# Optimization experiments

Hardware: AMD Instinct MI355X
Metric: run time of the kernel (lower is better)

The kernel has to match this reference:

```python
import jax, jax.numpy as jnp
import numpy as np

NUM_STEPS = 10
T0, T1 = 0.0, 1.0


def setup_inputs() -> dict:
    key = jax.random.key(0)
    ks = jax.random.split(key, 6)
    B, I, H = 4096, 1024, 2048
    sc_ih = 1.0 / np.sqrt(I)
    sc_hh = 1.0 / np.sqrt(H)
    return {
        "x": jax.random.normal(ks[0], (B, I), jnp.float32),
        "h0": jax.random.normal(ks[1], (B, H), jnp.float32),
        "W_ih": jax.random.normal(ks[2], (H, I), jnp.float32) * sc_ih,
        "b_ih": jax.random.normal(ks[3], (H,), jnp.float32) * sc_ih,
        "W_hh": jax.random.normal(ks[4], (H, H), jnp.float32) * sc_hh,
        "b_hh": jax.random.normal(ks[5], (H,), jnp.float32) * sc_hh,
        "tau": jnp.ones((H,), jnp.float32),
    }


def reference(x, h0, W_ih, b_ih, W_hh, b_hh, tau):
    dt = (T1 - T0) / NUM_STEPS
    # time-invariant input drive: W_ih(input) is the same every step
    ih = x @ W_ih.T + b_ih  # [B, H]
    decay = jnp.exp(-dt / tau)  # [H]

    def step(h, _):
        pre = ih + h @ W_hh.T + b_hh
        target = jnp.tanh(pre)
        h_new = decay * h + (1.0 - decay) * target
        return h_new, None

    h_final, _ = jax.lax.scan(step, h0, None, length=NUM_STEPS)
    return h_final
```

## Files before the change

### kernel.cpp

```cpp
#include <hip/hip_runtime.h>
#include <hip/hip_bf16.h>

#define NUM_STEPS 10
#define DT 0.1f

typedef __bf16 bf16_t;
typedef __bf16 bf16x8 __attribute__((ext_vector_type(8)));
typedef __bf16 bf16x4 __attribute__((ext_vector_type(4)));
typedef float f32x4 __attribute__((ext_vector_type(4)));

__device__ __forceinline__ void async16(const bf16_t* g, bf16_t* l) {
  __builtin_amdgcn_global_load_lds(
      (const __attribute__((address_space(1))) void*)g,
      (__attribute__((address_space(3))) void*)l, 16, 0, 0);
}

__global__ void cvt_f32_to_bf16(const float* __restrict__ in,
                                bf16_t* __restrict__ out, int n4) {
  int i = blockIdx.x * blockDim.x + threadIdx.x;
  if (i < n4) {
    float4 v = ((const float4*)in)[i];
    bf16x4 o = {(bf16_t)v.x, (bf16_t)v.y, (bf16_t)v.z, (bf16_t)v.w};
    ((bf16x4*)out)[i] = o;
  }
}

__global__ void make_decay(const float* __restrict__ tau,
                           float* __restrict__ decay, int n) {
  int i = blockIdx.x * blockDim.x + threadIdx.x;
  if (i < n) decay[i] = __expf(-DT / tau[i]);
}

template <int EPI>
__global__ __launch_bounds__(512, 2) void gemm_nt(
    const bf16_t* __restrict__ A, const bf16_t* __restrict__ Bw, int M, int N,
    int K, const float* __restrict__ bias1, const float* __restrict__ bias2,
    bf16_t* __restrict__ out_ihb, const bf16_t* __restrict__ ihb,
    const float* __restrict__ decay, const bf16_t* __restrict__ hb_prev,
    bf16_t* __restrict__ hb_next, float* __restrict__ out_f32, int writeOut) {
  extern __shared__ char smem[];

  const int tid = threadIdx.x;
  const int lane = tid & 63;
  const int wave = tid >> 6;
  const int waveM = wave >> 1;
  const int waveN = wave & 1;

  const int lin = blockIdx.y * gridDim.x + blockIdx.x;
  const int xcd = lin & 7;
  const int slot = lin >> 3;
  const int bx = (xcd & 1) * 8 + (slot & 7);
  const int by = (xcd >> 1) * 4 + (slot >> 3);
  const long bRow = (long)by * 256;
  const long bCol = (long)bx * 128;

  const int laneRow = lane & 15;
  const int laneK = (lane >> 4) << 3;
  const bf16_t* aG0 = A + (bRow + (wave * 2 + 0) * 16 + laneRow) * (long)K + laneK;
  const bf16_t* aG1 = A + (bRow + (wave * 2 + 1) * 16 + laneRow) * (long)K + laneK;
  const bf16_t* bG = Bw + (bCol + wave * 16 + laneRow) * (long)K + laneK;

  f32x4 acc[4][4] = {};

  auto stage = [&](int buf, int k0) {
    bf16_t* base = (bf16_t*)(smem + buf * 49152);
    async16(aG0 + k0, base + (wave * 2 + 0) * 1024);
    async16(aG0 + k0 + 32, base + (wave * 2 + 0) * 1024 + 512);
    async16(aG1 + k0, base + (wave * 2 + 1) * 1024);
    async16(aG1 + k0 + 32, base + (wave * 2 + 1) * 1024 + 512);
    async16(bG + k0, base + 16384 + wave * 1024);
    async16(bG + k0 + 32, base + 16384 + wave * 1024 + 512);
  };

  auto compute = [&](int buf) {
    const bf16_t* Ab = (const bf16_t*)(smem + buf * 49152);
    const bf16_t* Bb = Ab + 16384;
#pragma unroll
    for (int ks = 0; ks < 2; ++ks) {
      bf16x8 aF[4], bF[4];
#pragma unroll
      for (int t = 0; t < 4; ++t)
        aF[t] = *(const bf16x8*)&Ab[(waveM * 4 + t) * 1024 + ks * 512 + lane * 8];
#pragma unroll
      for (int u = 0; u < 4; ++u)
        bF[u] = *(const bf16x8*)&Bb[(waveN * 4 + u) * 1024 + ks * 512 + lane * 8];
      __builtin_amdgcn_s_setprio(1);
#pragma unroll
      for (int t = 0; t < 4; ++t)
#pragma unroll
        for (int u = 0; u < 4; ++u)
          acc[t][u] = __builtin_amdgcn_mfma_f32_16x16x32_bf16(aF[t], bF[u],
                                                              acc[t][u], 0, 0, 0);
      __builtin_amdgcn_s_setprio(0);
    }
  };

  const int NT = K >> 6;

  stage(0, 0);
  stage(1, 64);
  asm volatile("s_waitcnt vmcnt(6)" ::: "memory");
  __builtin_amdgcn_s_barrier();
  __builtin_amdgcn_sched_barrier(0);

  int cb = 0, sb = 2;
  for (int t = 0; t < NT - 2; ++t) {
    stage(sb, (t + 2) * 64);
    __builtin_amdgcn_sched_barrier(0);
    compute(cb);
    asm volatile("s_waitcnt lgkmcnt(0)" ::: "memory");
    asm volatile("s_waitcnt vmcnt(6)" ::: "memory");
    __builtin_amdgcn_s_barrier();
    __builtin_amdgcn_sched_barrier(0);
    cb = cb + 1; if (cb == 3) cb = 0;
    sb = sb + 1; if (sb == 3) sb = 0;
  }
  compute(cb);
  asm volatile("s_waitcnt lgkmcnt(0)" ::: "memory");
  asm volatile("s_waitcnt vmcnt(0)" ::: "memory");
  __builtin_amdgcn_s_barrier();
  __builtin_amdgcn_sched_barrier(0);
  cb = cb + 1; if (cb == 3) cb = 0;
  compute(cb);
  asm volatile("s_waitcnt lgkmcnt(0)" ::: "memory");
  __builtin_amdgcn_s_barrier();
  __builtin_amdgcn_sched_barrier(0);

  float* Ep = (float*)smem;
  const int eRow = (lane >> 4) << 2;
  const int eCol = lane & 15;
#pragma unroll
  for (int t = 0; t < 4; ++t)
#pragma unroll
    for (int u = 0; u < 4; ++u)
#pragma unroll
      for (int r = 0; r < 4; ++r) {
        const int rowL = waveM * 64 + t * 16 + eRow + r;
        const int colL = waveN * 64 + u * 16 + eCol;
        Ep[rowL * 128 + ((colL + 4 * rowL) & 127)] = acc[t][u][r];
      }
  asm volatile("s_waitcnt lgkmcnt(0)" ::: "memory");
  __builtin_amdgcn_s_barrier();
  __builtin_amdgcn_sched_barrier(0);

  const int rdRow = tid >> 3;
  const int col0 = (tid & 7) * 16;
#pragma unroll
  for (int p = 0; p < 4; ++p) {
    const int row = p * 64 + rdRow;
    float v[16];
#pragma unroll
    for (int c = 0; c < 4; ++c)
      *(f32x4*)&v[c * 4] =
          *(const f32x4*)&Ep[row * 128 + ((col0 + 4 * c + 4 * row) & 127)];
    const long g = (bRow + row) * (long)N + bCol + col0;

    if (EPI == 0) {
      f32x4 b1[4], b2[4];
#pragma unroll
      for (int c = 0; c < 4; ++c) {
        b1[c] = *(const f32x4*)&bias1[bCol + col0 + c * 4];
        b2[c] = *(const f32x4*)&bias2[bCol + col0 + c * 4];
      }
      bf16x8 o0, o1;
#pragma unroll
      for (int e = 0; e < 8; ++e)
        o0[e] = (bf16_t)(v[e] + b1[e >> 2][e & 3] + b2[e >> 2][e & 3]);
#pragma unroll
      for (int e = 0; e < 8; ++e)
        o1[e] = (bf16_t)(v[8 + e] + b1[2 + (e >> 2)][e & 3] +
                         b2[2 + (e >> 2)][e & 3]);
      *(bf16x8*)&out_ihb[g] = o0;
      *(bf16x8*)&out_ihb[g + 8] = o1;
    } else {
      const bf16x8 ih0 = *(const bf16x8*)&ihb[g];
      const bf16x8 ih1 = *(const bf16x8*)&ihb[g + 8];
      const bf16x8 hp0 = *(const bf16x8*)&hb_prev[g];
      const bf16x8 hp1 = *(const bf16x8*)&hb_prev[g + 8];
      f32x4 dc[4];
#pragma unroll
      for (int c = 0; c < 4; ++c)
        dc[c] = *(const f32x4*)&decay[bCol + col0 + c * 4];
      float hn[16];
      bf16x8 o0, o1;
#pragma unroll
      for (int e = 0; e < 8; ++e) {
        const float d = dc[e >> 2][e & 3];
        const float th = tanhf(v[e] + (float)ih0[e]);
        hn[e] = d * (float)hp0[e] + (1.0f - d) * th;
        o0[e] = (bf16_t)hn[e];
      }
#pragma unroll
      for (int e = 0; e < 8; ++e) {
        const float d = dc[2 + (e >> 2)][e & 3];
        const float th = tanhf(v[8 + e] + (float)ih1[e]);
        hn[8 + e] = d * (float)hp1[e] + (1.0f - d) * th;
        o1[e] = (bf16_t)hn[8 + e];
      }
      *(bf16x8*)&hb_next[g] = o0;
      *(bf16x8*)&hb_next[g + 8] = o1;
      if (writeOut) {
#pragma unroll
        for (int c = 0; c < 4; ++c)
          *(f32x4*)&out_f32[g + c * 4] = *(const f32x4*)&hn[c * 4];
      }
    }
  }
}

extern "C" void kernel_launch(void* const* d_in, const int* in_sizes, int n_in,
                              void* d_out, int out_size, void* d_ws,
                              size_t ws_size, hipStream_t stream) {
  const float* x = (const float*)d_in[0];
  const float* h0 = (const float*)d_in[1];
  const float* W_ih = (const float*)d_in[2];
  const float* b_ih = (const float*)d_in[3];
  const float* W_hh = (const float*)d_in[4];
  const float* b_hh = (const float*)d_in[5];
  const float* tau = (const float*)d_in[6];
  float* hout = (float*)d_out;

  const int B = 4096, I = 1024, H = 2048;

  char* ws = (char*)d_ws;
  bf16_t* ihb = (bf16_t*)ws; ws += (size_t)B * H * 2;
  bf16_t* hb0 = (bf16_t*)ws; ws += (size_t)B * H * 2;
  bf16_t* hb1 = (bf16_t*)ws; ws += (size_t)B * H * 2;
  bf16_t* xb = (bf16_t*)ws;  ws += (size_t)B * I * 2;
  bf16_t* wihb = (bf16_t*)ws; ws += (size_t)H * I * 2;
  bf16_t* whhb = (bf16_t*)ws; ws += (size_t)H * H * 2;
  float* decay = (float*)ws; ws += (size_t)H * 4;

  const int LDS_BYTES = 147456;
  (void)hipFuncSetAttribute(reinterpret_cast<const void*>(&gemm_nt<0>),
                            hipFuncAttributeMaxDynamicSharedMemorySize,
                            LDS_BYTES);
  (void)hipFuncSetAttribute(reinterpret_cast<const void*>(&gemm_nt<1>),
                            hipFuncAttributeMaxDynamicSharedMemorySize,
                            LDS_BYTES);

  cvt_f32_to_bf16<<<(B * I / 4 + 255) / 256, 256, 0, stream>>>(x, xb, B * I / 4);
  cvt_f32_to_bf16<<<(H * I / 4 + 255) / 256, 256, 0, stream>>>(W_ih, wihb, H * I / 4);
  cvt_f32_to_bf16<<<(H * H / 4 + 255) / 256, 256, 0, stream>>>(W_hh, whhb, H * H / 4);
  cvt_f32_to_bf16<<<(B * H / 4 + 255) / 256, 256, 0, stream>>>(h0, hb0, B * H / 4);
  make_decay<<<(H + 255) / 256, 256, 0, stream>>>(tau, decay, H);

  dim3 grid(H / 128, B / 256);
  gemm_nt<0><<<grid, 512, LDS_BYTES, stream>>>(
      xb, wihb, B, H, I, b_ih, b_hh, ihb, nullptr, nullptr, nullptr, nullptr,
      nullptr, 0);

  bf16_t* hb[2] = {hb0, hb1};
  for (int s = 0; s < NUM_STEPS; ++s) {
    gemm_nt<1><<<grid, 512, LDS_BYTES, stream>>>(
        hb[s & 1], whhb, B, H, H, nullptr, nullptr, nullptr, ihb, decay,
        hb[s & 1], hb[(s + 1) & 1], hout, (s == NUM_STEPS - 1) ? 1 : 0);
  }
}
```

Before: 735.9 us.

## Pre-swizzle operands into MFMA fragment layout and load directly from global

```diff
diff --git a/kernel.cpp b/kernel.cpp
--- a/kernel.cpp
+++ b/kernel.cpp
@@ -6,29 +6,30 @@
 
 typedef __bf16 bf16_t;
 typedef __bf16 bf16x8 __attribute__((ext_vector_type(8)));
-typedef __bf16 bf16x4 __attribute__((ext_vector_type(4)));
 typedef float f32x4 __attribute__((ext_vector_type(4)));
-
-__device__ __forceinline__ void async16(const bf16_t* g, bf16_t* l) {
-  __builtin_amdgcn_global_load_lds(
-      (const __attribute__((address_space(1))) void*)g,
-      (__attribute__((address_space(3))) void*)l, 16, 0, 0);
-}
-
-__global__ void cvt_f32_to_bf16(const float* __restrict__ in,
-                                bf16_t* __restrict__ out, int n4) {
-  int i = blockIdx.x * blockDim.x + threadIdx.x;
-  if (i < n4) {
-    float4 v = ((const float4*)in)[i];
-    bf16x4 o = {(bf16_t)v.x, (bf16_t)v.y, (bf16_t)v.z, (bf16_t)v.w};
-    ((bf16x4*)out)[i] = o;
-  }
-}
 
 __global__ void make_decay(const float* __restrict__ tau,
                            float* __restrict__ decay, int n) {
   int i = blockIdx.x * blockDim.x + threadIdx.x;
   if (i < n) decay[i] = __expf(-DT / tau[i]);
+}
+
+__global__ void cvt_swz(const float* __restrict__ in, bf16_t* __restrict__ out,
+                        int R, int Kd, int ksh) {
+  const long tid = (long)blockIdx.x * blockDim.x + threadIdx.x;
+  const long n = ((long)R * Kd) >> 3;
+  if (tid >= n) return;
+  const int slice = (int)(tid >> 6);
+  const int lane = (int)tid & 63;
+  const int g = slice >> ksh;
+  const int s = slice & ((1 << ksh) - 1);
+  const int r = (g << 4) + (lane & 15);
+  const int k = (s << 5) + ((lane >> 4) << 3);
+  const float4 v0 = *(const float4*)&in[(long)r * Kd + k];
+  const float4 v1 = *(const float4*)&in[(long)r * Kd + k + 4];
+  bf16x8 o = {(bf16_t)v0.x, (bf16_t)v0.y, (bf16_t)v0.z, (bf16_t)v0.w,
+              (bf16_t)v1.x, (bf16_t)v1.y, (bf16_t)v1.z, (bf16_t)v1.w};
+  *(bf16x8*)&out[tid << 3] = o;
 }
 
 template <int EPI>
@@ -48,100 +49,65 @@
 
   const int lin = blockIdx.y * gridDim.x + blockIdx.x;
   const int xcd = lin & 7;
-  const int slot = lin >> 3;
-  const int bx = (xcd & 1) * 8 + (slot & 7);
-  const int by = (xcd >> 1) * 4 + (slot >> 3);
+  const int slot_ = lin >> 3;
+  const int bx = (xcd & 1) * 8 + (slot_ & 7);
+  const int by = (xcd >> 1) * 4 + (slot_ >> 3);
   const long bRow = (long)by * 256;
   const long bCol = (long)bx * 128;
 
-  const int laneRow = lane & 15;
-  const int laneK = (lane >> 4) << 3;
-  const bf16_t* aG0 = A + (bRow + (wave * 2 + 0) * 16 + laneRow) * (long)K + laneK;
-  const bf16_t* aG1 = A + (bRow + (wave * 2 + 1) * 16 + laneRow) * (long)K + laneK;
-  const bf16_t* bG = Bw + (bCol + wave * 16 + laneRow) * (long)K + laneK;
+  const long KS = (long)K << 4;
+  const bf16_t* aP = A + ((long)((bRow >> 4) + waveM * 4)) * KS + (lane << 3);
+  const bf16_t* bP = Bw + ((long)((bCol >> 4) + waveN * 4)) * KS + (lane << 3);
 
   f32x4 acc[4][4] = {};
 
-  auto stage = [&](int buf, int k0) {
-    bf16_t* base = (bf16_t*)(smem + buf * 49152);
-    async16(aG0 + k0, base + (wave * 2 + 0) * 1024);
-    async16(aG0 + k0 + 32, base + (wave * 2 + 0) * 1024 + 512);
-    async16(aG1 + k0, base + (wave * 2 + 1) * 1024);
-    async16(aG1 + k0 + 32, base + (wave * 2 + 1) * 1024 + 512);
-    async16(bG + k0, base + 16384 + wave * 1024);
-    async16(bG + k0 + 32, base + 16384 + wave * 1024 + 512);
+  auto LD = [&](bf16x8 aF[4], bf16x8 bF[4], int s) {
+#pragma unroll
+    for (int i = 0; i < 4; ++i)
+      aF[i] = *(const bf16x8*)(aP + i * KS + ((long)s << 9));
+#pragma unroll
+    for (int u = 0; u < 4; ++u)
+      bF[u] = *(const bf16x8*)(bP + u * KS + ((long)s << 9));
   };
-
-  auto compute = [&](int buf) {
-    const bf16_t* Ab = (const bf16_t*)(smem + buf * 49152);
-    const bf16_t* Bb = Ab + 16384;
-#pragma unroll
-    for (int ks = 0; ks < 2; ++ks) {
-      bf16x8 aF[4], bF[4];
-#pragma unroll
-      for (int t = 0; t < 4; ++t)
-        aF[t] = *(const bf16x8*)&Ab[(waveM * 4 + t) * 1024 + ks * 512 + lane * 8];
+  auto FM = [&](const bf16x8 aF[4], const bf16x8 bF[4]) {
+#pragma unroll
+    for (int i = 0; i < 4; ++i)
 #pragma unroll
       for (int u = 0; u < 4; ++u)
-        bF[u] = *(const bf16x8*)&Bb[(waveN * 4 + u) * 1024 + ks * 512 + lane * 8];
-      __builtin_amdgcn_s_setprio(1);
-#pragma unroll
-      for (int t = 0; t < 4; ++t)
-#pragma unroll
-        for (int u = 0; u < 4; ++u)
-          acc[t][u] = __builtin_amdgcn_mfma_f32_16x16x32_bf16(aF[t], bF[u],
-                                                              acc[t][u], 0, 0, 0);
-      __builtin_amdgcn_s_setprio(0);
-    }
+        acc[i][u] = __builtin_amdgcn_mfma_f32_16x16x32_bf16(aF[i], bF[u],
+                                                            acc[i][u], 0, 0, 0);
   };
 
-  const int NT = K >> 6;
-
-  stage(0, 0);
-  stage(1, 64);
-  asm volatile("s_waitcnt vmcnt(6)" ::: "memory");
-  __builtin_amdgcn_s_barrier();
-  __builtin_amdgcn_sched_barrier(0);
-
-  int cb = 0, sb = 2;
-  for (int t = 0; t < NT - 2; ++t) {
-    stage(sb, (t + 2) * 64);
-    __builtin_amdgcn_sched_barrier(0);
-    compute(cb);
-    asm volatile("s_waitcnt lgkmcnt(0)" ::: "memory");
-    asm volatile("s_waitcnt vmcnt(6)" ::: "memory");
-    __builtin_amdgcn_s_barrier();
-    __builtin_amdgcn_sched_barrier(0);
-    cb = cb + 1; if (cb == 3) cb = 0;
-    sb = sb + 1; if (sb == 3) sb = 0;
-  }
-  compute(cb);
-  asm volatile("s_waitcnt lgkmcnt(0)" ::: "memory");
-  asm volatile("s_waitcnt vmcnt(0)" ::: "memory");
-  __builtin_amdgcn_s_barrier();
-  __builtin_amdgcn_sched_barrier(0);
-  cb = cb + 1; if (cb == 3) cb = 0;
-  compute(cb);
-  asm volatile("s_waitcnt lgkmcnt(0)" ::: "memory");
-  __builtin_amdgcn_s_barrier();
-  __builtin_amdgcn_sched_barrier(0);
+  const int NS = K >> 5;
+  bf16x8 a0[4], b0[4], a1[4], b1[4];
+  LD(a0, b0, 0);
+  int s = 0;
+  for (; s + 2 < NS; s += 2) {
+    LD(a1, b1, s + 1);
+    FM(a0, b0);
+    LD(a0, b0, s + 2);
+    FM(a1, b1);
+  }
+  LD(a1, b1, s + 1);
+  FM(a0, b0);
+  FM(a1, b1);
+
+  __syncthreads();
 
   float* Ep = (float*)smem;
   const int eRow = (lane >> 4) << 2;
   const int eCol = lane & 15;
 #pragma unroll
-  for (int t = 0; t < 4; ++t)
+  for (int i = 0; i < 4; ++i)
 #pragma unroll
     for (int u = 0; u < 4; ++u)
 #pragma unroll
       for (int r = 0; r < 4; ++r) {
-        const int rowL = waveM * 64 + t * 16 + eRow + r;
+        const int rowL = waveM * 64 + i * 16 + eRow + r;
         const int colL = waveN * 64 + u * 16 + eCol;
-        Ep[rowL * 128 + ((colL + 4 * rowL) & 127)] = acc[t][u][r];
-      }
-  asm volatile("s_waitcnt lgkmcnt(0)" ::: "memory");
-  __builtin_amdgcn_s_barrier();
-  __builtin_amdgcn_sched_barrier(0);
+        Ep[rowL * 128 + ((colL + 4 * rowL) & 127)] = acc[i][u][r];
+      }
+  __syncthreads();
 
   const int rdRow = tid >> 3;
   const int col0 = (tid & 7) * 16;
@@ -153,30 +119,38 @@
     for (int c = 0; c < 4; ++c)
       *(f32x4*)&v[c * 4] =
           *(const f32x4*)&Ep[row * 128 + ((col0 + 4 * c + 4 * row) & 127)];
-    const long g = (bRow + row) * (long)N + bCol + col0;
+    const long grow = bRow + row;
+    const long g = grow * (long)N + bCol + col0;
 
     if (EPI == 0) {
-      f32x4 b1[4], b2[4];
+      f32x4 b1v[4], b2v[4];
 #pragma unroll
       for (int c = 0; c < 4; ++c) {
-        b1[c] = *(const f32x4*)&bias1[bCol + col0 + c * 4];
-        b2[c] = *(const f32x4*)&bias2[bCol + col0 + c * 4];
+        b1v[c] = *(const f32x4*)&bias1[bCol + col0 + c * 4];
+        b2v[c] = *(const f32x4*)&bias2[bCol + col0 + c * 4];
       }
       bf16x8 o0, o1;
 #pragma unroll
       for (int e = 0; e < 8; ++e)
-        o0[e] = (bf16_t)(v[e] + b1[e >> 2][e & 3] + b2[e >> 2][e & 3]);
+        o0[e] = (bf16_t)(v[e] + b1v[e >> 2][e & 3] + b2v[e >> 2][e & 3]);
 #pragma unroll
       for (int e = 0; e < 8; ++e)
-        o1[e] = (bf16_t)(v[8 + e] + b1[2 + (e >> 2)][e & 3] +
-                         b2[2 + (e >> 2)][e & 3]);
+        o1[e] = (bf16_t)(v[8 + e] + b1v[2 + (e >> 2)][e & 3] +
+                         b2v[2 + (e >> 2)][e & 3]);
       *(bf16x8*)&out_ihb[g] = o0;
       *(bf16x8*)&out_ihb[g + 8] = o1;
     } else {
+      const long fg = (grow >> 4) * ((long)N >> 5);
+      const int s_ = (int)((bCol + col0) >> 5);
+      const int l0 = (row & 15) + (((col0 >> 3) + 0) & 3) * 16;
+      const int l1 = (row & 15) + (((col0 >> 3) + 1) & 3) * 16;
+      const long fo = (fg + s_) << 9;
+      const long o0a = fo + (l0 << 3);
+      const long o1a = fo + (l1 << 3);
       const bf16x8 ih0 = *(const bf16x8*)&ihb[g];
       const bf16x8 ih1 = *(const bf16x8*)&ihb[g + 8];
-      const bf16x8 hp0 = *(const bf16x8*)&hb_prev[g];
-      const bf16x8 hp1 = *(const bf16x8*)&hb_prev[g + 8];
+      const bf16x8 hp0 = *(const bf16x8*)&hb_prev[o0a];
+      const bf16x8 hp1 = *(const bf16x8*)&hb_prev[o1a];
       f32x4 dc[4];
 #pragma unroll
       for (int c = 0; c < 4; ++c)
@@ -197,8 +171,8 @@
         hn[8 + e] = d * (float)hp1[e] + (1.0f - d) * th;
         o1[e] = (bf16_t)hn[8 + e];
       }
-      *(bf16x8*)&hb_next[g] = o0;
-      *(bf16x8*)&hb_next[g + 8] = o1;
+      *(bf16x8*)&hb_next[o0a] = o0;
+      *(bf16x8*)&hb_next[o1a] = o1;
       if (writeOut) {
 #pragma unroll
         for (int c = 0; c < 4; ++c)
@@ -231,7 +205,7 @@
   bf16_t* whhb = (bf16_t*)ws; ws += (size_t)H * H * 2;
   float* decay = (float*)ws; ws += (size_t)H * 4;
 
-  const int LDS_BYTES = 147456;
+  const int LDS_BYTES = 131072;
   (void)hipFuncSetAttribute(reinterpret_cast<const void*>(&gemm_nt<0>),
                             hipFuncAttributeMaxDynamicSharedMemorySize,
                             LDS_BYTES);
@@ -239,10 +213,17 @@
                             hipFuncAttributeMaxDynamicSharedMemorySize,
                             LDS_BYTES);
 
-  cvt_f32_to_bf16<<<(B * I / 4 + 255) / 256, 256, 0, stream>>>(x, xb, B * I / 4);
-  cvt_f32_to_bf16<<<(H * I / 4 + 255) / 256, 256, 0, stream>>>(W_ih, wihb, H * I / 4);
-  cvt_f32_to_bf16<<<(H * H / 4 + 255) / 256, 256, 0, stream>>>(W_hh, whhb, H * H / 4);
-  cvt_f32_to_bf16<<<(B * H / 4 + 255) / 256, 256, 0, stream>>>(h0, hb0, B * H / 4);
+  {
+    long n;
+    n = (long)B * I / 8;
+    cvt_swz<<<(int)((n + 255) / 256), 256, 0, stream>>>(x, xb, B, I, 5);
+    n = (long)H * I / 8;
+    cvt_swz<<<(int)((n + 255) / 256), 256, 0, stream>>>(W_ih, wihb, H, I, 5);
+    n = (long)H * H / 8;
+    cvt_swz<<<(int)((n + 255) / 256), 256, 0, stream>>>(W_hh, whhb, H, H, 6);
+    n = (long)B * H / 8;
+    cvt_swz<<<(int)((n + 255) / 256), 256, 0, stream>>>(h0, hb0, B, H, 6);
+  }
   make_decay<<<(H + 255) / 256, 256, 0, stream>>>(tau, decay, H);
 
   dim3 grid(H / 128, B / 256);
```

Result: faster. 698.9 us (-5.0%).
